# Performance work log

Hardware: AMD Instinct MI355X
Metric: run time of the kernel (lower is better)

## Reference

```python
import jax, jax.numpy as jnp
import numpy as np

N_NODES = 100000
N_EDGES = 640000
NUM_GRAPHS = 256
IN_DIM, HID_DIM, OUT_DIM = 128, 128, 64


def setup_inputs() -> dict:
    key = jax.random.key(0)
    ks = jax.random.split(key, 6)
    x = jax.random.normal(ks[0], (N_NODES, IN_DIM), dtype=jnp.float32)
    edge_index = jax.random.randint(ks[1], (2, N_EDGES), 0, N_NODES, dtype=jnp.int64)
    batch = jnp.sort(jax.random.randint(ks[2], (N_NODES,), 0, NUM_GRAPHS, dtype=jnp.int64))
    W1 = jax.random.normal(ks[3], (IN_DIM, HID_DIM), dtype=jnp.float32) * (1.0 / np.sqrt(IN_DIM))
    b1 = jnp.zeros((HID_DIM,), dtype=jnp.float32)
    W2 = jax.random.normal(ks[4], (HID_DIM, OUT_DIM), dtype=jnp.float32) * (1.0 / np.sqrt(HID_DIM))
    b2 = jnp.zeros((OUT_DIM,), dtype=jnp.float32)
    return {"x": x, "edge_index": edge_index, "batch": batch,
            "W1": W1, "b1": b1, "W2": W2, "b2": b2}


def gcn_conv(x, row, col, norm, W, b, n_nodes):
    # transform first (smaller of in/out handled by W), then gather-scale-scatter
    xw = x @ W                                   # [N, F_out]
    msgs = norm[:, None] * xw[row]               # [E+N, F_out]
    out = jax.ops.segment_sum(msgs, col, num_segments=n_nodes)
    return out + b


def reference(x, edge_index, batch, W1, b1, W2, b2):
    n = x.shape[0]
    # add self-loops (PyG GCNConv default)
    loops = jnp.arange(n, dtype=edge_index.dtype)
    row = jnp.concatenate([edge_index[0], loops])  # sources
    col = jnp.concatenate([edge_index[1], loops])  # targets
    # symmetric normalization D^-1/2 (A+I) D^-1/2
    deg = jax.ops.segment_sum(jnp.ones_like(col, dtype=x.dtype), col, num_segments=n)
    dinv = jnp.where(deg > 0, jax.lax.rsqrt(deg), 0.0)
    norm = dinv[row] * dinv[col]
    h = jax.nn.relu(gcn_conv(x, row, col, norm, W1, b1, n))
    h = gcn_conv(h, row, col, norm, W2, b2, n)
    # global mean pool over batch ids
    sums = jax.ops.segment_sum(h, batch, num_segments=NUM_GRAPHS)
    counts = jax.ops.segment_sum(jnp.ones((n,), dtype=h.dtype), batch, num_segments=NUM_GRAPHS)
    return sums / jnp.clip(counts, 1.0)[:, None]
```

## Files before the change

### kernel.cpp

```cpp
#include <hip/hip_runtime.h>
#include <hip/hip_bf16.h>


typedef __attribute__((ext_vector_type(8))) short short8;
typedef __attribute__((ext_vector_type(4))) float f32x4;

__device__ __forceinline__ void atomAddF(float* p, float v) { unsafeAtomicAdd(p, v); }

__device__ __forceinline__ unsigned short bf_rne(float f) {
  unsigned int u = __float_as_uint(f);
  return (unsigned short)((u + 0x7fffu + ((u >> 16) & 1u)) >> 16);
}
__device__ __forceinline__ float bf2f(unsigned short h) {
  return __uint_as_float(((unsigned int)h) << 16);
}
__device__ __forceinline__ float bf_lo(unsigned int u) { return __uint_as_float(u << 16); }
__device__ __forceinline__ float bf_hi(unsigned int u) { return __uint_as_float(u & 0xffff0000u); }

__global__ __launch_bounds__(256) void k_prepx(const float* __restrict__ x,
                                               unsigned short* __restrict__ xb, long total8) {
  long i = (long)blockIdx.x * 256 + threadIdx.x;
  if (i >= total8) return;
  const float4* in = (const float4*)(x + i * 8);
  float4 a = in[0], b = in[1];
  short8 o;
  o[0] = (short)bf_rne(a.x); o[1] = (short)bf_rne(a.y);
  o[2] = (short)bf_rne(a.z); o[3] = (short)bf_rne(a.w);
  o[4] = (short)bf_rne(b.x); o[5] = (short)bf_rne(b.y);
  o[6] = (short)bf_rne(b.z); o[7] = (short)bf_rne(b.w);
  *(short8*)(xb + i * 8) = o;
}

__global__ __launch_bounds__(256) void k_prepw(const float* __restrict__ W1,
    const float* __restrict__ W2,
    unsigned short* __restrict__ W1th, unsigned short* __restrict__ W1tl,
    unsigned short* __restrict__ W2th, unsigned short* __restrict__ W2tl) {
  int i = blockIdx.x * 256 + threadIdx.x;
  if (i < 16384) {
    int c = i >> 7, k = i & 127;
    float f = W1[k * 128 + c];
    unsigned short hi = bf_rne(f);
    W1th[i] = hi;
    W1tl[i] = bf_rne(f - bf2f(hi));
  } else if (i < 16384 + 8192) {
    int j = i - 16384;
    int c = j >> 7, k = j & 127;
    float f = W2[k * 64 + c];
    unsigned short hi = bf_rne(f);
    W2th[j] = hi;
    W2tl[j] = bf_rne(f - bf2f(hi));
  }
}

__global__ __launch_bounds__(256) void k_count(const int* __restrict__ col,
                                               int* __restrict__ deg, int E) {
  int e = blockIdx.x * 256 + threadIdx.x;
  if (e < E) atomicAdd(&deg[col[e]], 1);
}

__global__ __launch_bounds__(256) void k_blocksum(const int* __restrict__ deg,
                                                  int* __restrict__ partial, int N) {
  __shared__ int sh[256];
  int t = threadIdx.x, i = blockIdx.x * 256 + t;
  sh[t] = (i < N) ? deg[i] : 0;
  __syncthreads();
  for (int o = 128; o > 0; o >>= 1) {
    if (t < o) sh[t] += sh[t + o];
    __syncthreads();
  }
  if (t == 0) partial[blockIdx.x] = sh[0];
}

__global__ __launch_bounds__(512) void k_scanpartial(int* __restrict__ partial, int nb) {
  __shared__ int sh[512];
  int t = threadIdx.x;
  int v = (t < nb) ? partial[t] : 0;
  sh[t] = v;
  __syncthreads();
  for (int o = 1; o < 512; o <<= 1) {
    int x = (t >= o) ? sh[t - o] : 0;
    __syncthreads();
    sh[t] += x;
    __syncthreads();
  }
  if (t < nb) partial[t] = sh[t] - v;
}

__global__ __launch_bounds__(256) void k_scanblock(int* __restrict__ deg,
    const int* __restrict__ partial, int* __restrict__ off,
    float* __restrict__ dinv, int N) {
  __shared__ int sh[256];
  int t = threadIdx.x, b = blockIdx.x, i = b * 256 + t;
  int v = (i < N) ? deg[i] : 0;
  sh[t] = v;
  __syncthreads();
  for (int o = 1; o < 256; o <<= 1) {
    int x = (t >= o) ? sh[t - o] : 0;
    __syncthreads();
    sh[t] += x;
    __syncthreads();
  }
  if (i < N) {
    int excl = partial[b] + sh[t] - v;
    off[i] = excl;
    deg[i] = excl;
    dinv[i] = rsqrtf((float)v + 1.0f);
    if (i == N - 1) off[N] = excl + v;
  }
}

__global__ __launch_bounds__(256) void k_fillcsr(const int* __restrict__ rows,
    const int* __restrict__ cols, int* __restrict__ cursor,
    int* __restrict__ csrsrc, int E) {
  int e = blockIdx.x * 256 + threadIdx.x;
  if (e < E) {
    int pos = atomicAdd(&cursor[cols[e]], 1);
    csrsrc[pos] = rows[e];
  }
}

__global__ __launch_bounds__(256) void k_goff(const int* __restrict__ batch,
                                              int* __restrict__ goff, int N, int G) {
  int g = blockIdx.x * 256 + threadIdx.x;
  if (g > G) return;
  int lo = 0, hi = N;
  while (lo < hi) {
    int m = (lo + hi) >> 1;
    if (batch[m] < g) lo = m + 1; else hi = m;
  }
  goff[g] = lo;
}

__global__ __launch_bounds__(256) void k_gemm1_mfma(
    const unsigned short* __restrict__ xb,
    const unsigned short* __restrict__ W1th, const unsigned short* __restrict__ W1tl,
    const float* __restrict__ dinv, unsigned short* __restrict__ yb, int N)
{
  const int tid = threadIdx.x;
  const int w = tid >> 6, l = tid & 63;
  const int v0 = blockIdx.x * 64;
  const int l15 = l & 15, lh = l >> 4;

  short8 bh[2][4], bl[2][4];
#pragma unroll
  for (int ct = 0; ct < 2; ++ct) {
    int colr = 32 * w + 16 * ct + l15;
#pragma unroll
    for (int ks = 0; ks < 4; ++ks) {
      bh[ct][ks] = *(const short8*)(W1th + colr * 128 + ks * 32 + 8 * lh);
      bl[ct][ks] = *(const short8*)(W1tl + colr * 128 + ks * 32 + 8 * lh);
    }
  }

  short8 af0_0, af0_1, af0_2, af0_3;
  short8 af1_0, af1_1, af1_2, af1_3;
  short8 af2_0, af2_1, af2_2, af2_3;
  short8 af3_0, af3_1, af3_2, af3_3;
  {
    int r0 = v0 + 0 * 16 + l15; if (r0 >= N) r0 = N - 1;
    int r1 = v0 + 1 * 16 + l15; if (r1 >= N) r1 = N - 1;
    int r2 = v0 + 2 * 16 + l15; if (r2 >= N) r2 = N - 1;
    int r3 = v0 + 3 * 16 + l15; if (r3 >= N) r3 = N - 1;
    const unsigned short* a0 = xb + (size_t)r0 * 128 + 8 * lh;
    const unsigned short* a1 = xb + (size_t)r1 * 128 + 8 * lh;
    const unsigned short* a2 = xb + (size_t)r2 * 128 + 8 * lh;
    const unsigned short* a3 = xb + (size_t)r3 * 128 + 8 * lh;
    af0_0 = *(const short8*)(a0);      af0_1 = *(const short8*)(a0 + 32);
    af0_2 = *(const short8*)(a0 + 64); af0_3 = *(const short8*)(a0 + 96);
    af1_0 = *(const short8*)(a1);      af1_1 = *(const short8*)(a1 + 32);
    af1_2 = *(const short8*)(a1 + 64); af1_3 = *(const short8*)(a1 + 96);
    af2_0 = *(const short8*)(a2);      af2_1 = *(const short8*)(a2 + 32);
    af2_2 = *(const short8*)(a2 + 64); af2_3 = *(const short8*)(a2 + 96);
    af3_0 = *(const short8*)(a3);      af3_1 = *(const short8*)(a3 + 32);
    af3_2 = *(const short8*)(a3 + 64); af3_3 = *(const short8*)(a3 + 96);
  }

#pragma unroll
  for (int rt = 0; rt < 4; ++rt) {
    short8 k0 = (rt == 0) ? af0_0 : (rt == 1) ? af1_0 : (rt == 2) ? af2_0 : af3_0;
    short8 k1 = (rt == 0) ? af0_1 : (rt == 1) ? af1_1 : (rt == 2) ? af2_1 : af3_1;
    short8 k2 = (rt == 0) ? af0_2 : (rt == 1) ? af1_2 : (rt == 2) ? af2_2 : af3_2;
    short8 k3 = (rt == 0) ? af0_3 : (rt == 1) ? af1_3 : (rt == 2) ? af2_3 : af3_3;
    f32x4 acc0 = {0.f, 0.f, 0.f, 0.f}, acc1 = {0.f, 0.f, 0.f, 0.f};
    acc0 = __builtin_amdgcn_mfma_f32_16x16x32_bf16(k0, bh[0][0], acc0, 0, 0, 0);
    acc1 = __builtin_amdgcn_mfma_f32_16x16x32_bf16(k0, bh[1][0], acc1, 0, 0, 0);
    acc0 = __builtin_amdgcn_mfma_f32_16x16x32_bf16(k0, bl[0][0], acc0, 0, 0, 0);
    acc1 = __builtin_amdgcn_mfma_f32_16x16x32_bf16(k0, bl[1][0], acc1, 0, 0, 0);
    acc0 = __builtin_amdgcn_mfma_f32_16x16x32_bf16(k1, bh[0][1], acc0, 0, 0, 0);
    acc1 = __builtin_amdgcn_mfma_f32_16x16x32_bf16(k1, bh[1][1], acc1, 0, 0, 0);
    acc0 = __builtin_amdgcn_mfma_f32_16x16x32_bf16(k1, bl[0][1], acc0, 0, 0, 0);
    acc1 = __builtin_amdgcn_mfma_f32_16x16x32_bf16(k1, bl[1][1], acc1, 0, 0, 0);
    acc0 = __builtin_amdgcn_mfma_f32_16x16x32_bf16(k2, bh[0][2], acc0, 0, 0, 0);
    acc1 = __builtin_amdgcn_mfma_f32_16x16x32_bf16(k2, bh[1][2], acc1, 0, 0, 0);
    acc0 = __builtin_amdgcn_mfma_f32_16x16x32_bf16(k2, bl[0][2], acc0, 0, 0, 0);
    acc1 = __builtin_amdgcn_mfma_f32_16x16x32_bf16(k2, bl[1][2], acc1, 0, 0, 0);
    acc0 = __builtin_amdgcn_mfma_f32_16x16x32_bf16(k3, bh[0][3], acc0, 0, 0, 0);
    acc1 = __builtin_amdgcn_mfma_f32_16x16x32_bf16(k3, bh[1][3], acc1, 0, 0, 0);
    acc0 = __builtin_amdgcn_mfma_f32_16x16x32_bf16(k3, bl[0][3], acc0, 0, 0, 0);
    acc1 = __builtin_amdgcn_mfma_f32_16x16x32_bf16(k3, bl[1][3], acc1, 0, 0, 0);

    int r4 = v0 + rt * 16 + lh * 4;
    float4 d4 = *(const float4*)(dinv + r4);
    int col0 = 32 * w + l15;
#pragma unroll
    for (int reg = 0; reg < 4; ++reg) {
      int row = r4 + reg;
      if (row < N) {
        float dd = (reg == 0) ? d4.x : (reg == 1) ? d4.y : (reg == 2) ? d4.z : d4.w;
        yb[(size_t)row * 128 + col0]      = bf_rne(acc0[reg] * dd);
        yb[(size_t)row * 128 + col0 + 16] = bf_rne(acc1[reg] * dd);
      }
    }
  }
}

__global__ __launch_bounds__(256, 4) void k_gemm2_fused_mfma(
    const unsigned short* __restrict__ yb, const int* __restrict__ off,
    const int* __restrict__ src,
    const unsigned short* __restrict__ W2th, const unsigned short* __restrict__ W2tl,
    const float* __restrict__ dinv, const float* __restrict__ b1,
    unsigned short* __restrict__ zb, int N)
{
  __shared__ __align__(16) unsigned short hh[32 * 128];
  __shared__ __align__(16) unsigned short hl[32 * 128];
  const int tid = threadIdx.x;
  const int w = tid >> 6, l = tid & 63;
  const int v0 = blockIdx.x * 32;
  const int l15 = l & 15, lh = l >> 4;

  {
    int vn = tid >> 3;
    int c0 = (tid & 7) << 4;
    int vv = v0 + vn;
    int vc = (vv < N) ? vv : N - 1;
    float acc[16];
    {
      const uint4* yr = (const uint4*)(yb + (size_t)vc * 128 + c0);
      uint4 t0 = yr[0], t1 = yr[1];
      acc[0]  = bf_lo(t0.x); acc[1]  = bf_hi(t0.x);
      acc[2]  = bf_lo(t0.y); acc[3]  = bf_hi(t0.y);
      acc[4]  = bf_lo(t0.z); acc[5]  = bf_hi(t0.z);
      acc[6]  = bf_lo(t0.w); acc[7]  = bf_hi(t0.w);
      acc[8]  = bf_lo(t1.x); acc[9]  = bf_hi(t1.x);
      acc[10] = bf_lo(t1.y); acc[11] = bf_hi(t1.y);
      acc[12] = bf_lo(t1.z); acc[13] = bf_hi(t1.z);
      acc[14] = bf_lo(t1.w); acc[15] = bf_hi(t1.w);
    }
    int e0 = off[vc], e1 = off[vc + 1];
    int last = e1 - 1;
    for (int i = e0; i < e1; i += 4) {
      int i1 = i + 1, i2 = i + 2, i3 = i + 3;
      int u0 = src[i];
      int u1 = src[i1 <= last ? i1 : last];
      int u2 = src[i2 <= last ? i2 : last];
      int u3 = src[i3 <= last ? i3 : last];
      float m1 = (i1 <= last) ? 1.f : 0.f;
      float m2 = (i2 <= last) ? 1.f : 0.f;
      float m3 = (i3 <= last) ? 1.f : 0.f;
      const uint4* p0 = (const uint4*)(yb + (size_t)u0 * 128 + c0);
      const uint4* p1 = (const uint4*)(yb + (size_t)u1 * 128 + c0);
      const uint4* p2 = (const uint4*)(yb + (size_t)u2 * 128 + c0);
      const uint4* p3 = (const uint4*)(yb + (size_t)u3 * 128 + c0);
      uint4 a0 = p0[0], b0 = p0[1];
      uint4 a1 = p1[0], b1v = p1[1];
      uint4 a2 = p2[0], b2v = p2[1];
      uint4 a3 = p3[0], b3v = p3[1];
      acc[0]  += bf_lo(a0.x) + m1*bf_lo(a1.x) + m2*bf_lo(a2.x) + m3*bf_lo(a3.x);
      acc[1]  += bf_hi(a0.x) + m1*bf_hi(a1.x) + m2*bf_hi(a2.x) + m3*bf_hi(a3.x);
      acc[2]  += bf_lo(a0.y) + m1*bf_lo(a1.y) + m2*bf_lo(a2.y) + m3*bf_lo(a3.y);
      acc[3]  += bf_hi(a0.y) + m1*bf_hi(a1.y) + m2*bf_hi(a2.y) + m3*bf_hi(a3.y);
      acc[4]  += bf_lo(a0.z) + m1*bf_lo(a1.z) + m2*bf_lo(a2.z) + m3*bf_lo(a3.z);
      acc[5]  += bf_hi(a0.z) + m1*bf_hi(a1.z) + m2*bf_hi(a2.z) + m3*bf_hi(a3.z);
      acc[6]  += bf_lo(a0.w) + m1*bf_lo(a1.w) + m2*bf_lo(a2.w) + m3*bf_lo(a3.w);
      acc[7]  += bf_hi(a0.w) + m1*bf_hi(a1.w) + m2*bf_hi(a2.w) + m3*bf_hi(a3.w);
      acc[8]  += bf_lo(b0.x) + m1*bf_lo(b1v.x) + m2*bf_lo(b2v.x) + m3*bf_lo(b3v.x);
      acc[9]  += bf_hi(b0.x) + m1*bf_hi(b1v.x) + m2*bf_hi(b2v.x) + m3*bf_hi(b3v.x);
      acc[10] += bf_lo(b0.y) + m1*bf_lo(b1v.y) + m2*bf_lo(b2v.y) + m3*bf_lo(b3v.y);
      acc[11] += bf_hi(b0.y) + m1*bf_hi(b1v.y) + m2*bf_hi(b2v.y) + m3*bf_hi(b3v.y);
      acc[12] += bf_lo(b0.z) + m1*bf_lo(b1v.z) + m2*bf_lo(b2v.z) + m3*bf_lo(b3v.z);
      acc[13] += bf_hi(b0.z) + m1*bf_hi(b1v.z) + m2*bf_hi(b2v.z) + m3*bf_hi(b3v.z);
      acc[14] += bf_lo(b0.w) + m1*bf_lo(b1v.w) + m2*bf_lo(b2v.w) + m3*bf_lo(b3v.w);
      acc[15] += bf_hi(b0.w) + m1*bf_hi(b1v.w) + m2*bf_hi(b2v.w) + m3*bf_hi(b3v.w);
    }
    float d = dinv[vc];
#pragma unroll
    for (int s = 0; s < 2; ++s) {
      short8 oh, ol;
#pragma unroll
      for (int j = 0; j < 8; ++j) {
        int dim = c0 + s * 8 + j;
        float hv = fmaxf(fmaf(d, acc[s*8+j], b1[dim]), 0.f);
        unsigned short hb = bf_rne(hv);
        oh[j] = (short)hb;
        ol[j] = (short)bf_rne(hv - bf2f(hb));
      }
      int byte = (vn * 256 + (c0 + s * 8) * 2) ^ ((vn & 7) << 4);
      *(short8*)((char*)hh + byte) = oh;
      *(short8*)((char*)hl + byte) = ol;
    }
  }

  short8 bh[4], bl[4];
  {
    int colr = 16 * w + l15;
#pragma unroll
    for (int ks = 0; ks < 4; ++ks) {
      bh[ks] = *(const short8*)(W2th + colr * 128 + ks * 32 + 8 * lh);
      bl[ks] = *(const short8*)(W2tl + colr * 128 + ks * 32 + 8 * lh);
    }
  }
  __syncthreads();

#pragma unroll
  for (int rt = 0; rt < 2; ++rt) {
    int row = rt * 16 + l15;
    const int swz = (row & 7) << 4;
    const int base = row * 256 + lh * 16;
    f32x4 acc = {0.f, 0.f, 0.f, 0.f};
#pragma unroll
    for (int ks = 0; ks < 4; ++ks) {
      int byte = (base + ks * 64) ^ swz;
      short8 ah = *(const short8*)((char*)hh + byte);
      short8 al = *(const short8*)((char*)hl + byte);
      acc = __builtin_amdgcn_mfma_f32_16x16x32_bf16(ah, bh[ks], acc, 0, 0, 0);
      acc = __builtin_amdgcn_mfma_f32_16x16x32_bf16(al, bh[ks], acc, 0, 0, 0);
      acc = __builtin_amdgcn_mfma_f32_16x16x32_bf16(ah, bl[ks], acc, 0, 0, 0);
    }

    int r4 = v0 + rt * 16 + lh * 4;
    float4 d4 = *(const float4*)(dinv + r4);
    int col = 16 * w + l15;
#pragma unroll
    for (int reg = 0; reg < 4; ++reg) {
      int rr = r4 + reg;
      if (rr < N) {
        float dd = (reg == 0) ? d4.x : (reg == 1) ? d4.y : (reg == 2) ? d4.z : d4.w;
        zb[(size_t)rr * 64 + col] = bf_rne(acc[reg] * dd);
      }
    }
  }
}

__global__ __launch_bounds__(256) void k_aggpool(
    const unsigned short* __restrict__ zb, const int* __restrict__ off,
    const int* __restrict__ src, const float* __restrict__ dinv,
    const int* __restrict__ goff, float* __restrict__ out, int N)
{
  int g = blockIdx.x >> 3, seg = blockIdx.x & 7;
  int w = threadIdx.x >> 6, lane = threadIdx.x & 63;
  int lo = goff[g], hi = goff[g + 1];
  float acc = 0.f;
  for (int v = lo + seg * 4 + w; v < hi; v += 32) {
    float sv = bf2f(zb[(size_t)v * 64 + lane]);
    int e0 = off[v], e1 = off[v + 1];
    int last = e1 - 1;
    for (int i = e0; i < e1; i += 4) {
      int i1 = i + 1, i2 = i + 2, i3 = i + 3;
      int u0 = src[i];
      int u1 = src[i1 <= last ? i1 : last];
      int u2 = src[i2 <= last ? i2 : last];
      int u3 = src[i3 <= last ? i3 : last];
      float a0 = bf2f(zb[(size_t)u0 * 64 + lane]);
      float a1 = bf2f(zb[(size_t)u1 * 64 + lane]);
      float a2 = bf2f(zb[(size_t)u2 * 64 + lane]);
      float a3 = bf2f(zb[(size_t)u3 * 64 + lane]);
      sv += a0;
      sv += (i1 <= last) ? a1 : 0.f;
      sv += (i2 <= last) ? a2 : 0.f;
      sv += (i3 <= last) ? a3 : 0.f;
    }
    acc = fmaf(dinv[v], sv, acc);
  }
  atomAddF(out + (size_t)g * 64 + lane, acc);
}

__global__ __launch_bounds__(256) void k_final(float* __restrict__ out,
    const int* __restrict__ goff, const float* __restrict__ b2, int total) {
  int i = blockIdx.x * 256 + threadIdx.x;
  if (i >= total) return;
  int g = i >> 6, d = i & 63;
  int n = goff[g + 1] - goff[g];
  out[i] = (n > 0) ? out[i] / (float)n + b2[d] : 0.f;
}

extern "C" void kernel_launch(void* const* d_in, const int* in_sizes, int n_in,
                              void* d_out, int out_size, void* d_ws, size_t ws_size,
                              hipStream_t stream) {
  const float* x     = (const float*)d_in[0];
  const int*   eidx  = (const int*)d_in[1];
  const int*   batch = (const int*)d_in[2];
  const float* W1    = (const float*)d_in[3];
  const float* b1    = (const float*)d_in[4];
  const float* W2    = (const float*)d_in[5];
  const float* b2    = (const float*)d_in[6];
  float* out = (float*)d_out;

  const int N = in_sizes[2];
  const int E = in_sizes[1] / 2;
  const int G = out_size / 64;

  const int* rows = eidx;
  const int* cols = eidx + E;

  unsigned short* xb  = (unsigned short*)d_ws;
  unsigned short* yb  = xb + (size_t)N * 128;
  unsigned short* zb  = yb + (size_t)N * 128;
  unsigned short* W1th = zb + (size_t)N * 64;
  unsigned short* W1tl = W1th + 16384;
  unsigned short* W2th = W1tl + 16384;
  unsigned short* W2tl = W2th + 8192;
  float* dinv    = (float*)(W2tl + 8192);
  int*   deg     = (int*)(dinv + N);
  int*   off     = deg + N;
  int*   partial = off + N + 1;
  int*   goff    = partial + 512;
  int*   csrsrc  = goff + G + 1;

  const int B = 256;
  const int nb = (N + B - 1) / B;

  hipMemsetAsync(deg, 0, (size_t)N * sizeof(int), stream);
  hipMemsetAsync(d_out, 0, (size_t)out_size * sizeof(float), stream);

  long total8 = (long)N * 16;
  k_prepx<<<(int)((total8 + B - 1) / B), B, 0, stream>>>(x, xb, total8);
  k_prepw<<<(16384 + 8192 + B - 1) / B, B, 0, stream>>>(W1, W2, W1th, W1tl, W2th, W2tl);

  k_count<<<(E + B - 1) / B, B, 0, stream>>>(cols, deg, E);
  k_blocksum<<<nb, B, 0, stream>>>(deg, partial, N);
  k_scanpartial<<<1, 512, 0, stream>>>(partial, nb);
  k_scanblock<<<nb, B, 0, stream>>>(deg, partial, off, dinv, N);
  k_fillcsr<<<(E + B - 1) / B, B, 0, stream>>>(rows, cols, deg, csrsrc, E);
  k_goff<<<(G + 1 + B - 1) / B, B, 0, stream>>>(batch, goff, N, G);

  k_gemm1_mfma<<<(N + 63) / 64, B, 0, stream>>>(xb, W1th, W1tl, dinv, yb, N);
  k_gemm2_fused_mfma<<<(N + 31) / 32, B, 0, stream>>>(yb, off, csrsrc, W2th, W2tl, dinv, b1, zb, N);
  k_aggpool<<<G * 8, B, 0, stream>>>(zb, off, csrsrc, dinv, goff, out, N);
  k_final<<<(out_size + B - 1) / B, B, 0, stream>>>(out, goff, b2, out_size);
}
```

Baseline: 290.6 us.

## Fuse preprocessing kernels into one cooperative kernel and split gather by halves

Replaces the two memsets and the eight preprocessing kernels (bf16 conversion, weight split, degree count, scans, CSR fill, graph offsets) with a single cooperative kernel of 512 blocks that separates its phases with grid.sync(), removing launch gaps. The cross-chunk scan becomes a serial loop run by one thread. Separately, the gather in gemm2 now makes two passes over 64-column halves with 8-way unrolled neighbour loads instead of one 128-column pass with 4-way unrolling. This doubles index reads but raises memory-level parallelism. Grid barriers and the serial scan add latency, and the cooperative launch needs all 512 blocks resident at once.

```diff
diff --git a/kernel.cpp b/kernel.cpp
--- a/kernel.cpp
+++ b/kernel.cpp
@@ -1,5 +1,8 @@
 #include <hip/hip_runtime.h>
 #include <hip/hip_bf16.h>
+#include <hip/hip_cooperative_groups.h>
+
+namespace cg = cooperative_groups;
 
 
 typedef __attribute__((ext_vector_type(8))) short short8;
@@ -17,118 +20,118 @@
 __device__ __forceinline__ float bf_lo(unsigned int u) { return __uint_as_float(u << 16); }
 __device__ __forceinline__ float bf_hi(unsigned int u) { return __uint_as_float(u & 0xffff0000u); }
 
-__global__ __launch_bounds__(256) void k_prepx(const float* __restrict__ x,
-                                               unsigned short* __restrict__ xb, long total8) {
-  long i = (long)blockIdx.x * 256 + threadIdx.x;
-  if (i >= total8) return;
-  const float4* in = (const float4*)(x + i * 8);
-  float4 a = in[0], b = in[1];
-  short8 o;
-  o[0] = (short)bf_rne(a.x); o[1] = (short)bf_rne(a.y);
-  o[2] = (short)bf_rne(a.z); o[3] = (short)bf_rne(a.w);
-  o[4] = (short)bf_rne(b.x); o[5] = (short)bf_rne(b.y);
-  o[6] = (short)bf_rne(b.z); o[7] = (short)bf_rne(b.w);
-  *(short8*)(xb + i * 8) = o;
-}
-
-__global__ __launch_bounds__(256) void k_prepw(const float* __restrict__ W1,
-    const float* __restrict__ W2,
+__global__ void k_build(
+    const float* __restrict__ x, const float* __restrict__ W1, const float* __restrict__ W2,
+    const int* __restrict__ rows, const int* __restrict__ cols, const int* __restrict__ batch,
+    unsigned short* __restrict__ xb,
     unsigned short* __restrict__ W1th, unsigned short* __restrict__ W1tl,
-    unsigned short* __restrict__ W2th, unsigned short* __restrict__ W2tl) {
-  int i = blockIdx.x * 256 + threadIdx.x;
-  if (i < 16384) {
-    int c = i >> 7, k = i & 127;
-    float f = W1[k * 128 + c];
-    unsigned short hi = bf_rne(f);
-    W1th[i] = hi;
-    W1tl[i] = bf_rne(f - bf2f(hi));
-  } else if (i < 16384 + 8192) {
-    int j = i - 16384;
-    int c = j >> 7, k = j & 127;
-    float f = W2[k * 64 + c];
-    unsigned short hi = bf_rne(f);
-    W2th[j] = hi;
-    W2tl[j] = bf_rne(f - bf2f(hi));
-  }
-}
-
-__global__ __launch_bounds__(256) void k_count(const int* __restrict__ col,
-                                               int* __restrict__ deg, int E) {
-  int e = blockIdx.x * 256 + threadIdx.x;
-  if (e < E) atomicAdd(&deg[col[e]], 1);
-}
-
-__global__ __launch_bounds__(256) void k_blocksum(const int* __restrict__ deg,
-                                                  int* __restrict__ partial, int N) {
+    unsigned short* __restrict__ W2th, unsigned short* __restrict__ W2tl,
+    int* __restrict__ deg, int* __restrict__ off, int* __restrict__ partial,
+    int* __restrict__ goff, int* __restrict__ csrsrc,
+    float* __restrict__ dinv, float* __restrict__ out,
+    int N, int E, int G)
+{
+  cg::grid_group grid = cg::this_grid();
+  const int tid = threadIdx.x;
+  const int gtid = blockIdx.x * 256 + tid;
+  const int nthr = gridDim.x * 256;
+  const int nch = (N + 255) >> 8;
   __shared__ int sh[256];
-  int t = threadIdx.x, i = blockIdx.x * 256 + t;
-  sh[t] = (i < N) ? deg[i] : 0;
-  __syncthreads();
-  for (int o = 128; o > 0; o >>= 1) {
-    if (t < o) sh[t] += sh[t + o];
-    __syncthreads();
-  }
-  if (t == 0) partial[blockIdx.x] = sh[0];
-}
-
-__global__ __launch_bounds__(512) void k_scanpartial(int* __restrict__ partial, int nb) {
-  __shared__ int sh[512];
-  int t = threadIdx.x;
-  int v = (t < nb) ? partial[t] : 0;
-  sh[t] = v;
-  __syncthreads();
-  for (int o = 1; o < 512; o <<= 1) {
-    int x = (t >= o) ? sh[t - o] : 0;
-    __syncthreads();
-    sh[t] += x;
-    __syncthreads();
-  }
-  if (t < nb) partial[t] = sh[t] - v;
-}
-
-__global__ __launch_bounds__(256) void k_scanblock(int* __restrict__ deg,
-    const int* __restrict__ partial, int* __restrict__ off,
-    float* __restrict__ dinv, int N) {
-  __shared__ int sh[256];
-  int t = threadIdx.x, b = blockIdx.x, i = b * 256 + t;
-  int v = (i < N) ? deg[i] : 0;
-  sh[t] = v;
-  __syncthreads();
-  for (int o = 1; o < 256; o <<= 1) {
-    int x = (t >= o) ? sh[t - o] : 0;
-    __syncthreads();
-    sh[t] += x;
-    __syncthreads();
-  }
-  if (i < N) {
-    int excl = partial[b] + sh[t] - v;
-    off[i] = excl;
-    deg[i] = excl;
-    dinv[i] = rsqrtf((float)v + 1.0f);
-    if (i == N - 1) off[N] = excl + v;
-  }
-}
-
-__global__ __launch_bounds__(256) void k_fillcsr(const int* __restrict__ rows,
-    const int* __restrict__ cols, int* __restrict__ cursor,
-    int* __restrict__ csrsrc, int E) {
-  int e = blockIdx.x * 256 + threadIdx.x;
-  if (e < E) {
-    int pos = atomicAdd(&cursor[cols[e]], 1);
+  __shared__ int sp[512];
+
+  {
+    long total8 = (long)N * 16;
+    for (long i = gtid; i < total8; i += nthr) {
+      const float4* in = (const float4*)(x + i * 8);
+      float4 a = in[0], b = in[1];
+      short8 o;
+      o[0] = (short)bf_rne(a.x); o[1] = (short)bf_rne(a.y);
+      o[2] = (short)bf_rne(a.z); o[3] = (short)bf_rne(a.w);
+      o[4] = (short)bf_rne(b.x); o[5] = (short)bf_rne(b.y);
+      o[6] = (short)bf_rne(b.z); o[7] = (short)bf_rne(b.w);
+      *(short8*)(xb + i * 8) = o;
+    }
+    for (int i = gtid; i < 16384 + 8192; i += nthr) {
+      if (i < 16384) {
+        int c = i >> 7, k = i & 127;
+        float f = W1[k * 128 + c];
+        unsigned short hi = bf_rne(f);
+        W1th[i] = hi; W1tl[i] = bf_rne(f - bf2f(hi));
+      } else {
+        int j = i - 16384;
+        int c = j >> 7, k = j & 127;
+        float f = W2[k * 64 + c];
+        unsigned short hi = bf_rne(f);
+        W2th[j] = hi; W2tl[j] = bf_rne(f - bf2f(hi));
+      }
+    }
+    for (int i = gtid; i < N; i += nthr) deg[i] = 0;
+    for (int i = gtid; i < G * 64; i += nthr) out[i] = 0.f;
+  }
+  grid.sync();
+
+  for (int e = gtid; e < E; e += nthr) atomicAdd(&deg[cols[e]], 1);
+  grid.sync();
+
+  for (int c = blockIdx.x; c < nch; c += gridDim.x) {
+    int i = c * 256 + tid;
+    sh[tid] = (i < N) ? deg[i] : 0;
+    __syncthreads();
+    for (int o = 128; o > 0; o >>= 1) {
+      if (tid < o) sh[tid] += sh[tid + o];
+      __syncthreads();
+    }
+    if (tid == 0) partial[c] = sh[0];
+    __syncthreads();
+  }
+  grid.sync();
+
+  if (blockIdx.x == 0) {
+    for (int i = tid; i < 512; i += 256) sp[i] = (i < nch) ? partial[i] : 0;
+    __syncthreads();
+    if (tid == 0) {
+      int run = 0;
+      for (int i = 0; i < nch; ++i) { int v = sp[i]; sp[i] = run; run += v; }
+    }
+    __syncthreads();
+    for (int i = tid; i < nch; i += 256) partial[i] = sp[i];
+  }
+  grid.sync();
+
+  for (int c = blockIdx.x; c < nch; c += gridDim.x) {
+    int i = c * 256 + tid;
+    int v = (i < N) ? deg[i] : 0;
+    sh[tid] = v;
+    __syncthreads();
+    for (int o = 1; o < 256; o <<= 1) {
+      int xval = (tid >= o) ? sh[tid - o] : 0;
+      __syncthreads();
+      sh[tid] += xval;
+      __syncthreads();
+    }
+    if (i < N) {
+      int excl = partial[c] + sh[tid] - v;
+      off[i] = excl;
+      deg[i] = excl;
+      dinv[i] = rsqrtf((float)v + 1.0f);
+      if (i == N - 1) off[N] = excl + v;
+    }
+    __syncthreads();
+  }
+  grid.sync();
+
+  for (int e = gtid; e < E; e += nthr) {
+    int pos = atomicAdd(&deg[cols[e]], 1);
     csrsrc[pos] = rows[e];
   }
-}
-
-__global__ __launch_bounds__(256) void k_goff(const int* __restrict__ batch,
-                                              int* __restrict__ goff, int N, int G) {
-  int g = blockIdx.x * 256 + threadIdx.x;
-  if (g > G) return;
-  int lo = 0, hi = N;
-  while (lo < hi) {
-    int m = (lo + hi) >> 1;
-    if (batch[m] < g) lo = m + 1; else hi = m;
-  }
-  goff[g] = lo;
+  for (int g = gtid; g <= G; g += nthr) {
+    int lo = 0, hi = N;
+    while (lo < hi) {
+      int m = (lo + hi) >> 1;
+      if (batch[m] < g) lo = m + 1; else hi = m;
+    }
+    goff[g] = lo;
+  }
 }
 
 __global__ __launch_bounds__(256) void k_gemm1_mfma(
@@ -230,71 +233,74 @@
 
   {
     int vn = tid >> 3;
-    int c0 = (tid & 7) << 4;
+    int d8 = (tid & 7) << 3;
     int vv = v0 + vn;
     int vc = (vv < N) ? vv : N - 1;
-    float acc[16];
-    {
-      const uint4* yr = (const uint4*)(yb + (size_t)vc * 128 + c0);
-      uint4 t0 = yr[0], t1 = yr[1];
-      acc[0]  = bf_lo(t0.x); acc[1]  = bf_hi(t0.x);
-      acc[2]  = bf_lo(t0.y); acc[3]  = bf_hi(t0.y);
-      acc[4]  = bf_lo(t0.z); acc[5]  = bf_hi(t0.z);
-      acc[6]  = bf_lo(t0.w); acc[7]  = bf_hi(t0.w);
-      acc[8]  = bf_lo(t1.x); acc[9]  = bf_hi(t1.x);
-      acc[10] = bf_lo(t1.y); acc[11] = bf_hi(t1.y);
-      acc[12] = bf_lo(t1.z); acc[13] = bf_hi(t1.z);
-      acc[14] = bf_lo(t1.w); acc[15] = bf_hi(t1.w);
-    }
     int e0 = off[vc], e1 = off[vc + 1];
     int last = e1 - 1;
-    for (int i = e0; i < e1; i += 4) {
-      int i1 = i + 1, i2 = i + 2, i3 = i + 3;
-      int u0 = src[i];
-      int u1 = src[i1 <= last ? i1 : last];
-      int u2 = src[i2 <= last ? i2 : last];
-      int u3 = src[i3 <= last ? i3 : last];
-      float m1 = (i1 <= last) ? 1.f : 0.f;
-      float m2 = (i2 <= last) ? 1.f : 0.f;
-      float m3 = (i3 <= last) ? 1.f : 0.f;
-      const uint4* p0 = (const uint4*)(yb + (size_t)u0 * 128 + c0);
-      const uint4* p1 = (const uint4*)(yb + (size_t)u1 * 128 + c0);
-      const uint4* p2 = (const uint4*)(yb + (size_t)u2 * 128 + c0);
-      const uint4* p3 = (const uint4*)(yb + (size_t)u3 * 128 + c0);
-      uint4 a0 = p0[0], b0 = p0[1];
-      uint4 a1 = p1[0], b1v = p1[1];
-      uint4 a2 = p2[0], b2v = p2[1];
-      uint4 a3 = p3[0], b3v = p3[1];
-      acc[0]  += bf_lo(a0.x) + m1*bf_lo(a1.x) + m2*bf_lo(a2.x) + m3*bf_lo(a3.x);
-      acc[1]  += bf_hi(a0.x) + m1*bf_hi(a1.x) + m2*bf_hi(a2.x) + m3*bf_hi(a3.x);
-      acc[2]  += bf_lo(a0.y) + m1*bf_lo(a1.y) + m2*bf_lo(a2.y) + m3*bf_lo(a3.y);
-      acc[3]  += bf_hi(a0.y) + m1*bf_hi(a1.y) + m2*bf_hi(a2.y) + m3*bf_hi(a3.y);
-      acc[4]  += bf_lo(a0.z) + m1*bf_lo(a1.z) + m2*bf_lo(a2.z) + m3*bf_lo(a3.z);
-      acc[5]  += bf_hi(a0.z) + m1*bf_hi(a1.z) + m2*bf_hi(a2.z) + m3*bf_hi(a3.z);
-      acc[6]  += bf_lo(a0.w) + m1*bf_lo(a1.w) + m2*bf_lo(a2.w) + m3*bf_lo(a3.w);
-      acc[7]  += bf_hi(a0.w) + m1*bf_hi(a1.w) + m2*bf_hi(a2.w) + m3*bf_hi(a3.w);
-      acc[8]  += bf_lo(b0.x) + m1*bf_lo(b1v.x) + m2*bf_lo(b2v.x) + m3*bf_lo(b3v.x);
-      acc[9]  += bf_hi(b0.x) + m1*bf_hi(b1v.x) + m2*bf_hi(b2v.x) + m3*bf_hi(b3v.x);
-      acc[10] += bf_lo(b0.y) + m1*bf_lo(b1v.y) + m2*bf_lo(b2v.y) + m3*bf_lo(b3v.y);
-      acc[11] += bf_hi(b0.y) + m1*bf_hi(b1v.y) + m2*bf_hi(b2v.y) + m3*bf_hi(b3v.y);
-      acc[12] += bf_lo(b0.z) + m1*bf_lo(b1v.z) + m2*bf_lo(b2v.z) + m3*bf_lo(b3v.z);
-      acc[13] += bf_hi(b0.z) + m1*bf_hi(b1v.z) + m2*bf_hi(b2v.z) + m3*bf_hi(b3v.z);
-      acc[14] += bf_lo(b0.w) + m1*bf_lo(b1v.w) + m2*bf_lo(b2v.w) + m3*bf_lo(b3v.w);
-      acc[15] += bf_hi(b0.w) + m1*bf_hi(b1v.w) + m2*bf_hi(b2v.w) + m3*bf_hi(b3v.w);
-    }
     float d = dinv[vc];
 #pragma unroll
-    for (int s = 0; s < 2; ++s) {
+    for (int ph = 0; ph < 2; ++ph) {
+      int cd = ph * 64 + d8;
+      float acc[8];
+      {
+        uint4 t = *(const uint4*)(yb + (size_t)vc * 128 + cd);
+        acc[0] = bf_lo(t.x); acc[1] = bf_hi(t.x);
+        acc[2] = bf_lo(t.y); acc[3] = bf_hi(t.y);
+        acc[4] = bf_lo(t.z); acc[5] = bf_hi(t.z);
+        acc[6] = bf_lo(t.w); acc[7] = bf_hi(t.w);
+      }
+      for (int i = e0; i < e1; i += 8) {
+        int i1 = i + 1, i2 = i + 2, i3 = i + 3, i4 = i + 4, i5 = i + 5, i6 = i + 6, i7 = i + 7;
+        int u0 = src[i];
+        int u1 = src[i1 <= last ? i1 : last];
+        int u2 = src[i2 <= last ? i2 : last];
+        int u3 = src[i3 <= last ? i3 : last];
+        int u4 = src[i4 <= last ? i4 : last];
+        int u5 = src[i5 <= last ? i5 : last];
+        int u6 = src[i6 <= last ? i6 : last];
+        int u7 = src[i7 <= last ? i7 : last];
+        float m1 = (i1 <= last) ? 1.f : 0.f;
+        float m2 = (i2 <= last) ? 1.f : 0.f;
+        float m3 = (i3 <= last) ? 1.f : 0.f;
+        float m4 = (i4 <= last) ? 1.f : 0.f;
+        float m5 = (i5 <= last) ? 1.f : 0.f;
+        float m6 = (i6 <= last) ? 1.f : 0.f;
+        float m7 = (i7 <= last) ? 1.f : 0.f;
+        uint4 t0 = *(const uint4*)(yb + (size_t)u0 * 128 + cd);
+        uint4 t1 = *(const uint4*)(yb + (size_t)u1 * 128 + cd);
+        uint4 t2 = *(const uint4*)(yb + (size_t)u2 * 128 + cd);
+        uint4 t3 = *(const uint4*)(yb + (size_t)u3 * 128 + cd);
+        uint4 t4 = *(const uint4*)(yb + (size_t)u4 * 128 + cd);
+        uint4 t5 = *(const uint4*)(yb + (size_t)u5 * 128 + cd);
+        uint4 t6 = *(const uint4*)(yb + (size_t)u6 * 128 + cd);
+        uint4 t7 = *(const uint4*)(yb + (size_t)u7 * 128 + cd);
+        acc[0] += bf_lo(t0.x) + m1*bf_lo(t1.x) + m2*bf_lo(t2.x) + m3*bf_lo(t3.x)
+                + m4*bf_lo(t4.x) + m5*bf_lo(t5.x) + m6*bf_lo(t6.x) + m7*bf_lo(t7.x);
+        acc[1] += bf_hi(t0.x) + m1*bf_hi(t1.x) + m2*bf_hi(t2.x) + m3*bf_hi(t3.x)
+                + m4*bf_hi(t4.x) + m5*bf_hi(t5.x) + m6*bf_hi(t6.x) + m7*bf_hi(t7.x);
+        acc[2] += bf_lo(t0.y) + m1*bf_lo(t1.y) + m2*bf_lo(t2.y) + m3*bf_lo(t3.y)
+                + m4*bf_lo(t4.y) + m5*bf_lo(t5.y) + m6*bf_lo(t6.y) + m7*bf_lo(t7.y);
+        acc[3] += bf_hi(t0.y) + m1*bf_hi(t1.y) + m2*bf_hi(t2.y) + m3*bf_hi(t3.y)
+                + m4*bf_hi(t4.y) + m5*bf_hi(t5.y) + m6*bf_hi(t6.y) + m7*bf_hi(t7.y);
+        acc[4] += bf_lo(t0.z) + m1*bf_lo(t1.z) + m2*bf_lo(t2.z) + m3*bf_lo(t3.z)
+                + m4*bf_lo(t4.z) + m5*bf_lo(t5.z) + m6*bf_lo(t6.z) + m7*bf_lo(t7.z);
+        acc[5] += bf_hi(t0.z) + m1*bf_hi(t1.z) + m2*bf_hi(t2.z) + m3*bf_hi(t3.z)
+                + m4*bf_hi(t4.z) + m5*bf_hi(t5.z) + m6*bf_hi(t6.z) + m7*bf_hi(t7.z);
+        acc[6] += bf_lo(t0.w) + m1*bf_lo(t1.w) + m2*bf_lo(t2.w) + m3*bf_lo(t3.w)
+                + m4*bf_lo(t4.w) + m5*bf_lo(t5.w) + m6*bf_lo(t6.w) + m7*bf_lo(t7.w);
+        acc[7] += bf_hi(t0.w) + m1*bf_hi(t1.w) + m2*bf_hi(t2.w) + m3*bf_hi(t3.w)
+                + m4*bf_hi(t4.w) + m5*bf_hi(t5.w) + m6*bf_hi(t6.w) + m7*bf_hi(t7.w);
+      }
       short8 oh, ol;
 #pragma unroll
       for (int j = 0; j < 8; ++j) {
-        int dim = c0 + s * 8 + j;
-        float hv = fmaxf(fmaf(d, acc[s*8+j], b1[dim]), 0.f);
+        float hv = fmaxf(fmaf(d, acc[j], b1[cd + j]), 0.f);
         unsigned short hb = bf_rne(hv);
         oh[j] = (short)hb;
         ol[j] = (short)bf_rne(hv - bf2f(hb));
       }
-      int byte = (vn * 256 + (c0 + s * 8) * 2) ^ ((vn & 7) << 4);
+      int byte = (vn * 256 + cd * 2) ^ ((vn & 7) << 4);
       *(short8*)((char*)hh + byte) = oh;
       *(short8*)((char*)hl + byte) = ol;
     }
@@ -417,21 +423,23 @@
   int*   csrsrc  = goff + G + 1;
 
   const int B = 256;
-  const int nb = (N + B - 1) / B;
-
-  hipMemsetAsync(deg, 0, (size_t)N * sizeof(int), stream);
-  hipMemsetAsync(d_out, 0, (size_t)out_size * sizeof(float), stream);
-
-  long total8 = (long)N * 16;
-  k_prepx<<<(int)((total8 + B - 1) / B), B, 0, stream>>>(x, xb, total8);
-  k_prepw<<<(16384 + 8192 + B - 1) / B, B, 0, stream>>>(W1, W2, W1th, W1tl, W2th, W2tl);
-
-  k_count<<<(E + B - 1) / B, B, 0, stream>>>(cols, deg, E);
-  k_blocksum<<<nb, B, 0, stream>>>(deg, partial, N);
-  k_scanpartial<<<1, 512, 0, stream>>>(partial, nb);
-  k_scanblock<<<nb, B, 0, stream>>>(deg, partial, off, dinv, N);
-  k_fillcsr<<<(E + B - 1) / B, B, 0, stream>>>(rows, cols, deg, csrsrc, E);
-  k_goff<<<(G + 1 + B - 1) / B, B, 0, stream>>>(batch, goff, N, G);
+
+  {
+    void* kb_x = (void*)x; void* kb_W1 = (void*)W1; void* kb_W2 = (void*)W2;
+    void* kb_rows = (void*)rows; void* kb_cols = (void*)cols; void* kb_batch = (void*)batch;
+    void* kb_xb = (void*)xb;
+    void* kb_W1th = (void*)W1th; void* kb_W1tl = (void*)W1tl;
+    void* kb_W2th = (void*)W2th; void* kb_W2tl = (void*)W2tl;
+    void* kb_deg = (void*)deg; void* kb_off = (void*)off; void* kb_partial = (void*)partial;
+    void* kb_goff = (void*)goff; void* kb_csrsrc = (void*)csrsrc;
+    void* kb_dinv = (void*)dinv; void* kb_out = (void*)out;
+    int nN = N, nE = E, nG = G;
+    void* args[] = { &kb_x, &kb_W1, &kb_W2, &kb_rows, &kb_cols, &kb_batch,
+                     &kb_xb, &kb_W1th, &kb_W1tl, &kb_W2th, &kb_W2tl,
+                     &kb_deg, &kb_off, &kb_partial, &kb_goff, &kb_csrsrc,
+                     &kb_dinv, &kb_out, &nN, &nE, &nG };
+    hipLaunchCooperativeKernel((const void*)k_build, dim3(512), dim3(B), args, 0, stream);
+  }
 
   k_gemm1_mfma<<<(N + 63) / 64, B, 0, stream>>>(xb, W1th, W1tl, dinv, yb, N);
   k_gemm2_fused_mfma<<<(N + 31) / 32, B, 0, stream>>>(yb, off, csrsrc, W2th, W2tl, dinv, b1, zb, N);
```

Result: slower. 596.2 us (+105.1%).
